# Kernel tuning notes

Hardware: AMD Instinct MI355X
Metric: run time of the kernel (lower is better)

## Reference

```python
import jax, jax.numpy as jnp
import numpy as np

N_NODES = 50000
N_EDGES = 800000
NODE_DIM = 10
EDGE_DIM = 5
HID = 64


def _tconv(x, src, dst, e_attr, wq, bq, wk, bk, wv, bv, we, ws, bs):
    # PyG TransformerConv, heads=1, concat=True, root_weight=True, beta=False
    n = x.shape[0]
    q = x @ wq + bq                      # [N, HID]
    k = x @ wk + bk                      # [N, HID]
    v = x @ wv + bv                      # [N, HID]
    ee = e_attr @ we                     # [E, HID] (lin_edge, no bias)
    ke = k[src] + ee                     # key per edge
    ve = v[src] + ee                     # value per edge
    logits = jnp.sum(q[dst] * ke, axis=-1) / 8.0  # sqrt(64) = 8
    m = jax.ops.segment_max(logits, dst, num_segments=n)
    p = jnp.exp(logits - m[dst])
    s = jax.ops.segment_sum(p, dst, num_segments=n)
    alpha = p / s[dst]                   # segment softmax over in-neighbors
    agg = jax.ops.segment_sum(alpha[:, None] * ve, dst, num_segments=n)
    return agg + x @ ws + bs             # + lin_skip(x_i)


def setup_inputs() -> dict:
    key = jax.random.key(0)
    ks = jax.random.split(key, 32)
    x = jax.random.uniform(ks[0], (N_NODES, NODE_DIM), dtype=jnp.float32)
    edge_index = jax.random.randint(ks[1], (2, N_EDGES), 0, N_NODES, dtype=jnp.int64)
    edge_attr = jax.random.uniform(ks[2], (N_EDGES, EDGE_DIM), dtype=jnp.float32)

    def lin(k, fan_in, fan_out):
        b = 1.0 / np.sqrt(fan_in)
        return jax.random.uniform(k, (fan_in, fan_out), jnp.float32, -b, b)

    def bias(k, fan_in, fan_out):
        b = 1.0 / np.sqrt(fan_in)
        return jax.random.uniform(k, (fan_out,), jnp.float32, -b, b)

    inp = dict(x=x, edge_index=edge_index, edge_attr=edge_attr)
    # conv1: NODE_DIM -> HID
    inp['w1q'] = lin(ks[3], NODE_DIM, HID); inp['b1q'] = bias(ks[4], NODE_DIM, HID)
    inp['w1k'] = lin(ks[5], NODE_DIM, HID); inp['b1k'] = bias(ks[6], NODE_DIM, HID)
    inp['w1v'] = lin(ks[7], NODE_DIM, HID); inp['b1v'] = bias(ks[8], NODE_DIM, HID)
    inp['w1e'] = lin(ks[9], EDGE_DIM, HID)
    inp['w1s'] = lin(ks[10], NODE_DIM, HID); inp['b1s'] = bias(ks[11], NODE_DIM, HID)
    # 5 stacked HID -> HID layers
    inp['wq'] = jnp.stack([lin(jax.random.fold_in(ks[12], i), HID, HID) for i in range(5)])
    inp['bq'] = jnp.stack([bias(jax.random.fold_in(ks[13], i), HID, HID) for i in range(5)])
    inp['wk'] = jnp.stack([lin(jax.random.fold_in(ks[14], i), HID, HID) for i in range(5)])
    inp['bk'] = jnp.stack([bias(jax.random.fold_in(ks[15], i), HID, HID) for i in range(5)])
    inp['wv'] = jnp.stack([lin(jax.random.fold_in(ks[16], i), HID, HID) for i in range(5)])
    inp['bv'] = jnp.stack([bias(jax.random.fold_in(ks[17], i), HID, HID) for i in range(5)])
    inp['we'] = jnp.stack([lin(jax.random.fold_in(ks[18], i), EDGE_DIM, HID) for i in range(5)])
    inp['ws'] = jnp.stack([lin(jax.random.fold_in(ks[19], i), HID, HID) for i in range(5)])
    inp['bs'] = jnp.stack([bias(jax.random.fold_in(ks[20], i), HID, HID) for i in range(5)])
    # final linear HID -> 1
    inp['lin_w'] = lin(ks[21], HID, 1); inp['lin_b'] = bias(ks[22], HID, 1)
    return inp


def reference(x, edge_index, edge_attr, w1q, b1q, w1k, b1k, w1v, b1v, w1e, w1s, b1s,
              wq, bq, wk, bk, wv, bv, we, ws, bs, lin_w, lin_b):
    src, dst = edge_index[0], edge_index[1]  # x_j = x[src], aggregated into dst
    h = jnp.log(x + 1.0)
    e = jnp.log(edge_attr + 1.0)
    h = _tconv(h, src, dst, e, w1q, b1q, w1k, b1k, w1v, b1v, w1e, w1s, b1s)
    for i in range(5):
        h = _tconv(h, src, dst, e, wq[i], bq[i], wk[i], bk[i], wv[i], bv[i], we[i], ws[i], bs[i])
    return h @ lin_w + lin_b  # [N, 1]
```

## Files before the change

### kernel.cpp

```cpp
#include <hip/hip_runtime.h>
#include <hip/hip_fp16.h>
#include <cstdint>
#include <cstddef>

#define NN 50000
#define NE 800000
#define HD 64
#define SB 49
#define NT64 6250

__global__ void k_hist(const int* __restrict__ ei, int* __restrict__ cnt) {
    int e = blockIdx.x * blockDim.x + threadIdx.x;
    if (e < NE) atomicAdd(&cnt[ei[NE + e]], 1);
}

__global__ __launch_bounds__(256) void k_scan1(const int* __restrict__ cnt,
                                               int* __restrict__ row_start,
                                               int* __restrict__ bsum) {
    __shared__ int ssum[256];
    const int tid = threadIdx.x, b = blockIdx.x;
    const int i0 = b * 1024 + tid * 4;
    int c0 = 0, c1 = 0, c2 = 0, c3 = 0;
    if (i0 + 3 < NN) {
        const int4 c = *(const int4*)(cnt + i0);
        c0 = c.x; c1 = c.y; c2 = c.z; c3 = c.w;
    } else {
        if (i0 + 0 < NN) c0 = cnt[i0 + 0];
        if (i0 + 1 < NN) c1 = cnt[i0 + 1];
        if (i0 + 2 < NN) c2 = cnt[i0 + 2];
        if (i0 + 3 < NN) c3 = cnt[i0 + 3];
    }
    ssum[tid] = c0 + c1 + c2 + c3;
    __syncthreads();
    for (int off = 1; off < 256; off <<= 1) {
        int v = (tid >= off) ? ssum[tid - off] : 0;
        __syncthreads();
        ssum[tid] += v;
        __syncthreads();
    }
    int ex = (tid == 0) ? 0 : ssum[tid - 1];
    if (i0 + 0 < NN) row_start[i0 + 0] = ex;
    ex += c0;
    if (i0 + 1 < NN) row_start[i0 + 1] = ex;
    ex += c1;
    if (i0 + 2 < NN) row_start[i0 + 2] = ex;
    ex += c2;
    if (i0 + 3 < NN) row_start[i0 + 3] = ex;
    if (tid == 255) bsum[b] = ssum[255];
}

__global__ __launch_bounds__(64) void k_scan2(const int* __restrict__ bsum,
                                              int* __restrict__ boff,
                                              int* __restrict__ row_start) {
    __shared__ int s[64];
    const int t = threadIdx.x;
    s[t] = (t < SB) ? bsum[t] : 0;
    __syncthreads();
    for (int off = 1; off < 64; off <<= 1) {
        int v = (t >= off) ? s[t - off] : 0;
        __syncthreads();
        s[t] += v;
        __syncthreads();
    }
    if (t < SB) boff[t] = (t == 0) ? 0 : s[t - 1];
    if (t == 0) row_start[NN] = s[SB - 1];
}

__global__ __launch_bounds__(256) void k_scan3(int* __restrict__ row_start,
                                               const int* __restrict__ boff,
                                               int* __restrict__ cur) {
    const int b = blockIdx.x;
    const int i0 = b * 1024 + threadIdx.x * 4;
    const int o = boff[b];
#pragma unroll
    for (int k = 0; k < 4; ++k) {
        int i = i0 + k;
        if (i < NN) {
            int v = row_start[i] + o;
            row_start[i] = v;
            cur[i] = v;
        }
    }
}

__global__ void k_scatter(const int* __restrict__ ei, const float* __restrict__ ea,
                          int* __restrict__ cur, uint4* __restrict__ e5p) {
    int e = blockIdx.x * blockDim.x + threadIdx.x;
    if (e < NE) {
        int d = ei[NE + e];
        int pos = atomicAdd(&cur[d], 1);
        const float e0 = __logf(ea[e * 5 + 0] + 1.f);
        const float e1 = __logf(ea[e * 5 + 1] + 1.f);
        const float e2 = __logf(ea[e * 5 + 2] + 1.f);
        const float e3 = __logf(ea[e * 5 + 3] + 1.f);
        const float e4 = __logf(ea[e * 5 + 4] + 1.f);
        union { __half2 h; unsigned u; } c01, c23;
        c01.h = __floats2half2_rn(e0, e1);
        c23.h = __floats2half2_rn(e2, e3);
        uint4 rec;
        rec.x = c01.u;
        rec.y = c23.u;
        rec.z = ((unsigned)ei[e] << 16) |
                (unsigned)__half_as_ushort(__float2half_rn(e4));
        rec.w = 0u;
        e5p[pos] = rec;
    }
}

__device__ __forceinline__ void cvt_kv(const uint4 u, float4& k4, float4& v4) {
    const float2 p0 = __half22float2(*(const __half2*)&u.x);
    const float2 p1 = __half22float2(*(const __half2*)&u.y);
    const float2 p2 = __half22float2(*(const __half2*)&u.z);
    const float2 p3 = __half22float2(*(const __half2*)&u.w);
    k4 = make_float4(p0.x, p1.x, p2.x, p3.x);
    v4 = make_float4(p0.y, p1.y, p2.y, p3.y);
}

__global__ __launch_bounds__(256, 4) void k_qkvs64(
    const float* __restrict__ h,
    const float* __restrict__ Wq, const float* __restrict__ Bq,
    const float* __restrict__ Wk, const float* __restrict__ Bk,
    const float* __restrict__ Wv, const float* __restrict__ Bv,
    const float* __restrict__ Ws, const float* __restrict__ Bs,
    float* __restrict__ qb, __half* __restrict__ kvh, float* __restrict__ sb) {
    __shared__ float xs[2][512];
    __shared__ float kls[512];
    const int lane = threadIdx.x & 63;
    const int w = threadIdx.x >> 6;
    const float* W = (w == 0) ? Wq : (w == 1) ? Ws : (w == 2) ? Wk : Wv;
    const float* B = (w == 0) ? Bq : (w == 1) ? Bs : (w == 2) ? Bk : Bv;
    const float scl = (w == 0) ? 0.125f : 1.f;
    float wr[64];
#pragma unroll
    for (int j = 0; j < 64; ++j) wr[j] = W[j * 64 + lane] * scl;
    const float bias = B[lane] * scl;

    int tile = blockIdx.x;
    {
        const float2 g = *(const float2*)(h + (size_t)tile * 512 + threadIdx.x * 2);
        *(float2*)&xs[0][threadIdx.x * 2] = g;
    }
    __syncthreads();
    int buf = 0;
    while (true) {
        const int nt = tile + gridDim.x;
        const bool more = nt < NT64;
        float2 gn;
        if (more) gn = *(const float2*)(h + (size_t)nt * 512 + threadIdx.x * 2);
        float acc[8] = {bias, bias, bias, bias, bias, bias, bias, bias};
#pragma unroll
        for (int jq = 0; jq < 16; ++jq) {
#pragma unroll
            for (int n = 0; n < 8; ++n) {
                const float4 xv = *(const float4*)&xs[buf][n * 64 + jq * 4];
                acc[n] = fmaf(xv.x, wr[jq * 4 + 0], acc[n]);
                acc[n] = fmaf(xv.y, wr[jq * 4 + 1], acc[n]);
                acc[n] = fmaf(xv.z, wr[jq * 4 + 2], acc[n]);
                acc[n] = fmaf(xv.w, wr[jq * 4 + 3], acc[n]);
            }
        }
        if (w == 2) {
#pragma unroll
            for (int n = 0; n < 8; ++n) kls[n * 64 + lane] = acc[n];
        }
        if (more) *(float2*)&xs[buf ^ 1][threadIdx.x * 2] = gn;
        __syncthreads();
        const int nb = tile * 8;
        if (w == 0) {
#pragma unroll
            for (int n = 0; n < 8; ++n) qb[(size_t)(nb + n) * 64 + lane] = acc[n];
        } else if (w == 1) {
#pragma unroll
            for (int n = 0; n < 8; ++n) sb[(size_t)(nb + n) * 64 + lane] = acc[n];
        } else if (w == 3) {
#pragma unroll
            for (int n = 0; n < 8; ++n) {
                const float kk = kls[n * 64 + lane];
                *(__half2*)(kvh + (size_t)(nb + n) * 128 + lane * 2) =
                    __floats2half2_rn(kk, acc[n]);
            }
        }
        if (!more) break;
        __syncthreads();
        tile = nt;
        buf ^= 1;
    }
}

__global__ __launch_bounds__(256, 4) void k_qkvs10(
    const float* __restrict__ x,
    const float* __restrict__ Wq, const float* __restrict__ Bq,
    const float* __restrict__ Wk, const float* __restrict__ Bk,
    const float* __restrict__ Wv, const float* __restrict__ Bv,
    const float* __restrict__ Ws, const float* __restrict__ Bs,
    float* __restrict__ qb, __half* __restrict__ kvh, float* __restrict__ sb) {
    __shared__ float xs[640];
    const int lane = threadIdx.x & 63;
    const int w = threadIdx.x >> 6;
    const bool iskv = (w == 1 || w == 3);
    const float* WA = (w == 0) ? Wq : iskv ? Wk : Ws;
    const float* BA = (w == 0) ? Bq : iskv ? Bk : Bs;
    const float scl = (w == 0) ? 0.125f : 1.f;
    float wrA[10], wrB[10];
#pragma unroll
    for (int j = 0; j < 10; ++j) {
        wrA[j] = WA[j * 64 + lane] * scl;
        wrB[j] = iskv ? Wv[j * 64 + lane] : 0.f;
    }
    const float bA = BA[lane] * scl;
    const float bB = iskv ? Bv[lane] : 0.f;
    const int tile = blockIdx.x;
    const int fbase = tile * 640;
    const int fcnt = min(640, NN * 10 - fbase);
    if (threadIdx.x * 4 < fcnt) {
        float4 v = *(const float4*)(x + (size_t)fbase + threadIdx.x * 4);
        v.x = __logf(v.x + 1.f);
        v.y = __logf(v.y + 1.f);
        v.z = __logf(v.z + 1.f);
        v.w = __logf(v.w + 1.f);
        *(float4*)&xs[threadIdx.x * 4] = v;
    }
    __syncthreads();
    const int nbase = tile * 64;
    const int nodes = min(64, NN - nbase);
    const int n0 = (w == 3) ? 32 : 0;
    const int n1 = iskv ? ((w == 1) ? min(nodes, 32) : nodes) : nodes;
    for (int n = n0; n < n1; ++n) {
        float accA = bA, accB = bB;
#pragma unroll
        for (int j = 0; j < 10; ++j) {
            const float xv = xs[n * 10 + j];
            accA = fmaf(xv, wrA[j], accA);
            accB = fmaf(xv, wrB[j], accB);
        }
        const size_t node = (size_t)(nbase + n);
        if (iskv) {
            const __half2 hv = __floats2half2_rn(accA, accB);
            *(__half2*)(kvh + node * 128 + lane * 2) = hv;
        } else if (w == 0) {
            qb[node * 64 + lane] = accA;
        } else {
            sb[node * 64 + lane] = accA;
        }
    }
}

template <bool FINAL>
__global__ __launch_bounds__(256) void k_agg(
    const float* __restrict__ q, const __half* __restrict__ kv,
    const float* __restrict__ sk, const uint4* __restrict__ e5p,
    const float* __restrict__ wE, const int* __restrict__ row_start,
    float* __restrict__ hout, const float* __restrict__ lw, const float* lb) {
    const int lane = threadIdx.x & 63;
    const int g = lane >> 4, t = lane & 15;
    const int node = __builtin_amdgcn_readfirstlane(blockIdx.x * 4 + (threadIdx.x >> 6));
    if (node >= NN) return;
    const int beg = row_start[node], end = row_start[node + 1];
    if (beg == end) {
        const float4 s4 = *(const float4*)(sk + (size_t)node * 64 + t * 4);
        if (FINAL) {
            const float4 lw4 = *(const float4*)(lw + t * 4);
            float r = s4.x * lw4.x;
            r = fmaf(s4.y, lw4.y, r);
            r = fmaf(s4.z, lw4.z, r);
            r = fmaf(s4.w, lw4.w, r);
            r += __shfl_xor(r, 1);
            r += __shfl_xor(r, 2);
            r += __shfl_xor(r, 4);
            r += __shfl_xor(r, 8);
            if (lane == 0) hout[node] = r + lb[0];
        } else if (g == 0) {
            *(float4*)(hout + (size_t)node * 64 + t * 4) = s4;
        }
        return;
    }
    const float4 q4 = *(const float4*)(q + (size_t)node * 64 + t * 4);
    float g5[5];
    {
        const float4 wg = *(const float4*)(wE + g * 64 + t * 4);
        float dc = q4.x * wg.x;
        dc = fmaf(q4.y, wg.y, dc);
        dc = fmaf(q4.z, wg.z, dc);
        dc = fmaf(q4.w, wg.w, dc);
        dc += __shfl_xor(dc, 1);
        dc += __shfl_xor(dc, 2);
        dc += __shfl_xor(dc, 4);
        dc += __shfl_xor(dc, 8);
        const float4 w4 = *(const float4*)(wE + 4 * 64 + t * 4);
        float d4 = q4.x * w4.x;
        d4 = fmaf(q4.y, w4.y, d4);
        d4 = fmaf(q4.z, w4.z, d4);
        d4 = fmaf(q4.w, w4.w, d4);
        d4 += __shfl_xor(d4, 1);
        d4 += __shfl_xor(d4, 2);
        d4 += __shfl_xor(d4, 4);
        d4 += __shfl_xor(d4, 8);
        g5[0] = __shfl(dc, 0);
        g5[1] = __shfl(dc, 16);
        g5[2] = __shfl(dc, 32);
        g5[3] = __shfl(dc, 48);
        g5[4] = __shfl(d4, 0);
    }
    float m = -1e30f, l = 0.f;
    float4 accv = {0.f, 0.f, 0.f, 0.f};
    float a50 = 0.f, a51 = 0.f, a52 = 0.f, a53 = 0.f, a54 = 0.f;
    const char* kvc = (const char*)kv;
    const int i0x = beg + g;
    const int i0 = (i0x < end) ? i0x : beg;
    uint4 r0 = e5p[i0];
    const int i1x = beg + 4 + g;
    const int i1 = (i1x < end) ? i1x : beg;
    uint4 r1 = e5p[i1];
    uint4 kv8 =
        *(const uint4*)(kvc + (size_t)((r0.z & 0xffff0000u) >> 8) + t * 16);
#pragma unroll 2
    for (int p = beg; p < end; p += 4) {
        const int nx = p + 8 + g;
        const int npp = (nx < end) ? nx : beg;
        const uint4 rn = e5p[npp];
        const uint4 nkv =
            *(const uint4*)(kvc + (size_t)((r1.z & 0xffff0000u) >> 8) + t * 16);
        const bool act = (p + g) < end;
        float4 k4, v4;
        cvt_kv(kv8, k4, v4);
        const float2 e01 = __half22float2(*(const __half2*)&r0.x);
        const float2 e23 = __half22float2(*(const __half2*)&r0.y);
        const float e4v =
            __half2float(__ushort_as_half((unsigned short)(r0.z & 0xffffu)));
        float d = q4.x * k4.x;
        d = fmaf(q4.y, k4.y, d);
        d = fmaf(q4.z, k4.z, d);
        d = fmaf(q4.w, k4.w, d);
        d += __shfl_xor(d, 1);
        d += __shfl_xor(d, 2);
        d += __shfl_xor(d, 4);
        d += __shfl_xor(d, 8);
        float d5 = g5[0] * e01.x;
        d5 = fmaf(g5[1], e01.y, d5);
        d5 = fmaf(g5[2], e23.x, d5);
        d5 = fmaf(g5[3], e23.y, d5);
        d5 = fmaf(g5[4], e4v, d5);
        const float la = act ? (d + d5) : -1e30f;
        const float nm = fmaxf(m, la);
        const float scl = __expf(m - nm);
        const float pa = __expf(la - nm);
        l = fmaf(l, scl, pa);
        accv.x = fmaf(accv.x, scl, pa * v4.x);
        accv.y = fmaf(accv.y, scl, pa * v4.y);
        accv.z = fmaf(accv.z, scl, pa * v4.z);
        accv.w = fmaf(accv.w, scl, pa * v4.w);
        a50 = fmaf(a50, scl, pa * e01.x);
        a51 = fmaf(a51, scl, pa * e01.y);
        a52 = fmaf(a52, scl, pa * e23.x);
        a53 = fmaf(a53, scl, pa * e23.y);
        a54 = fmaf(a54, scl, pa * e4v);
        m = nm;
        r0 = r1;
        r1 = rn;
        kv8 = nkv;
    }
    float M = fmaxf(m, __shfl_xor(m, 16));
    M = fmaxf(M, __shfl_xor(M, 32));
    const float f = __expf(m - M);
    float lz = l * f;
    lz += __shfl_xor(lz, 16);
    lz += __shfl_xor(lz, 32);
    accv.x *= f;
    accv.y *= f;
    accv.z *= f;
    accv.w *= f;
    a50 *= f;
    a51 *= f;
    a52 *= f;
    a53 *= f;
    a54 *= f;
#pragma unroll
    for (int s = 16; s <= 32; s <<= 1) {
        accv.x += __shfl_xor(accv.x, s);
        accv.y += __shfl_xor(accv.y, s);
        accv.z += __shfl_xor(accv.z, s);
        accv.w += __shfl_xor(accv.w, s);
        a50 += __shfl_xor(a50, s);
        a51 += __shfl_xor(a51, s);
        a52 += __shfl_xor(a52, s);
        a53 += __shfl_xor(a53, s);
        a54 += __shfl_xor(a54, s);
    }
    float4 t4 = accv;
    {
        const float4 w0 = *(const float4*)(wE + 0 * 64 + t * 4);
        const float4 w1 = *(const float4*)(wE + 1 * 64 + t * 4);
        const float4 w2 = *(const float4*)(wE + 2 * 64 + t * 4);
        const float4 w3 = *(const float4*)(wE + 3 * 64 + t * 4);
        const float4 w4r = *(const float4*)(wE + 4 * 64 + t * 4);
        t4.x = fmaf(a50, w0.x, t4.x);
        t4.y = fmaf(a50, w0.y, t4.y);
        t4.z = fmaf(a50, w0.z, t4.z);
        t4.w = fmaf(a50, w0.w, t4.w);
        t4.x = fmaf(a51, w1.x, t4.x);
        t4.y = fmaf(a51, w1.y, t4.y);
        t4.z = fmaf(a51, w1.z, t4.z);
        t4.w = fmaf(a51, w1.w, t4.w);
        t4.x = fmaf(a52, w2.x, t4.x);
        t4.y = fmaf(a52, w2.y, t4.y);
        t4.z = fmaf(a52, w2.z, t4.z);
        t4.w = fmaf(a52, w2.w, t4.w);
        t4.x = fmaf(a53, w3.x, t4.x);
        t4.y = fmaf(a53, w3.y, t4.y);
        t4.z = fmaf(a53, w3.z, t4.z);
        t4.w = fmaf(a53, w3.w, t4.w);
        t4.x = fmaf(a54, w4r.x, t4.x);
        t4.y = fmaf(a54, w4r.y, t4.y);
        t4.z = fmaf(a54, w4r.z, t4.z);
        t4.w = fmaf(a54, w4r.w, t4.w);
    }
    const float4 s4 = *(const float4*)(sk + (size_t)node * 64 + t * 4);
    const float rl = 1.f / lz;
    float4 o;
    o.x = fmaf(t4.x, rl, s4.x);
    o.y = fmaf(t4.y, rl, s4.y);
    o.z = fmaf(t4.z, rl, s4.z);
    o.w = fmaf(t4.w, rl, s4.w);
    if (FINAL) {
        const float4 lw4 = *(const float4*)(lw + t * 4);
        float r = o.x * lw4.x;
        r = fmaf(o.y, lw4.y, r);
        r = fmaf(o.z, lw4.z, r);
        r = fmaf(o.w, lw4.w, r);
        r += __shfl_xor(r, 1);
        r += __shfl_xor(r, 2);
        r += __shfl_xor(r, 4);
        r += __shfl_xor(r, 8);
        if (lane == 0) hout[node] = r + lb[0];
    } else if (g == 0) {
        *(float4*)(hout + (size_t)node * 64 + t * 4) = o;
    }
}

extern "C" void kernel_launch(void* const* d_in, const int* in_sizes, int n_in,
                              void* d_out, int out_size, void* d_ws, size_t ws_size,
                              hipStream_t stream) {
    const float* x = (const float*)d_in[0];
    const int* ei = (const int*)d_in[1];
    const float* ea = (const float*)d_in[2];
    const float* w1q = (const float*)d_in[3];
    const float* b1q = (const float*)d_in[4];
    const float* w1k = (const float*)d_in[5];
    const float* b1k = (const float*)d_in[6];
    const float* w1v = (const float*)d_in[7];
    const float* b1v = (const float*)d_in[8];
    const float* w1e = (const float*)d_in[9];
    const float* w1s = (const float*)d_in[10];
    const float* b1s = (const float*)d_in[11];
    const float* wq = (const float*)d_in[12];
    const float* bq = (const float*)d_in[13];
    const float* wk = (const float*)d_in[14];
    const float* bk = (const float*)d_in[15];
    const float* wv = (const float*)d_in[16];
    const float* bv = (const float*)d_in[17];
    const float* we = (const float*)d_in[18];
    const float* ws = (const float*)d_in[19];
    const float* bs = (const float*)d_in[20];
    const float* lw = (const float*)d_in[21];
    const float* lb = (const float*)d_in[22];

    uintptr_t p = (uintptr_t)d_ws;
    auto alloc = [&](size_t bytes) -> void* {
        void* r = (void*)p;
        p += (bytes + 255) & ~(size_t)255;
        return r;
    };
    uint4* e5p = (uint4*)alloc((size_t)NE * 16);
    float* hb = (float*)alloc((size_t)NN * HD * 4);
    __half* kvh = (__half*)alloc((size_t)NN * 128 * 2);
    float* qb = (float*)alloc((size_t)NN * HD * 4);
    float* sb = (float*)alloc((size_t)NN * HD * 4);
    int* row_start = (int*)alloc((size_t)(NN + 1) * 4);
    int* cnt = (int*)alloc((size_t)NN * 4);
    int* cur = (int*)alloc((size_t)NN * 4);
    int* bsum = (int*)alloc((size_t)SB * 4);
    int* boff = (int*)alloc((size_t)SB * 4);

    hipMemsetAsync(cnt, 0, (size_t)NN * 4, stream);
    k_hist<<<(NE + 255) / 256, 256, 0, stream>>>(ei, cnt);
    k_scan1<<<SB, 256, 0, stream>>>(cnt, row_start, bsum);
    k_scan2<<<1, 64, 0, stream>>>(bsum, boff, row_start);
    k_scan3<<<SB, 256, 0, stream>>>(row_start, boff, cur);
    k_scatter<<<(NE + 255) / 256, 256, 0, stream>>>(ei, ea, cur, e5p);

    const int gg64 = 1024;
    const int gg10 = (NN + 63) / 64;
    const int agg_grid = (NN + 3) / 4;

    k_qkvs10<<<gg10, 256, 0, stream>>>(x, w1q, b1q, w1k, b1k, w1v, b1v, w1s, b1s,
                                       qb, kvh, sb);
    k_agg<false><<<agg_grid, 256, 0, stream>>>(qb, kvh, sb, e5p, w1e, row_start,
                                               hb, lw, lb);

    for (int i = 0; i < 5; ++i) {
        k_qkvs64<<<gg64, 256, 0, stream>>>(hb, wq + i * 4096, bq + i * 64,
                                           wk + i * 4096, bk + i * 64,
                                           wv + i * 4096, bv + i * 64,
                                           ws + i * 4096, bs + i * 64,
                                           qb, kvh, sb);
        if (i < 4) {
            k_agg<false><<<agg_grid, 256, 0, stream>>>(qb, kvh, sb, e5p,
                                                       we + i * 320, row_start, hb,
                                                       lw, lb);
        } else {
            k_agg<true><<<agg_grid, 256, 0, stream>>>(qb, kvh, sb, e5p,
                                                      we + i * 320, row_start,
                                                      (float*)d_out, lw, lb);
        }
    }
}
```

Measured before the change: 640.8 us.

## Process eight edges per wave in aggregation and split CSR build into perm+pack

The aggregation kernel now splits each 64-lane wave into 8 groups of 8 lanes, each lane handling 8 feature channels, instead of 4 groups of 16 lanes with 4 channels. Each wave therefore processes 8 edges per iteration with wider per-lane loads and one fewer shuffle stage. The CSR construction is also restructured: edge records are computed in the histogram pass, the scatter writes only a permutation index, and a separate pack kernel gathers the records. This adds an extra 12.8MB temp buffer and two extra passes over edges, and raises register pressure in the aggregation loop.

Measured after the change: 702.4 us. +9.6%, slower.

```diff
diff --git a/kernel.cpp b/kernel.cpp
--- a/kernel.cpp
+++ b/kernel.cpp
@@ -9,9 +9,27 @@
 #define SB 49
 #define NT64 6250
 
-__global__ void k_hist(const int* __restrict__ ei, int* __restrict__ cnt) {
+__global__ void k_histprep(const int* __restrict__ ei, const float* __restrict__ ea,
+                           int* __restrict__ cnt, uint4* __restrict__ tmp) {
     int e = blockIdx.x * blockDim.x + threadIdx.x;
-    if (e < NE) atomicAdd(&cnt[ei[NE + e]], 1);
+    if (e < NE) {
+        atomicAdd(&cnt[ei[NE + e]], 1);
+        const float e0 = __logf(ea[e * 5 + 0] + 1.f);
+        const float e1 = __logf(ea[e * 5 + 1] + 1.f);
+        const float e2 = __logf(ea[e * 5 + 2] + 1.f);
+        const float e3 = __logf(ea[e * 5 + 3] + 1.f);
+        const float e4 = __logf(ea[e * 5 + 4] + 1.f);
+        union { __half2 h; unsigned u; } c01, c23;
+        c01.h = __floats2half2_rn(e0, e1);
+        c23.h = __floats2half2_rn(e2, e3);
+        uint4 rec;
+        rec.x = c01.u;
+        rec.y = c23.u;
+        rec.z = ((unsigned)ei[e] << 16) |
+                (unsigned)__half_as_ushort(__float2half_rn(e4));
+        rec.w = 0u;
+        tmp[e] = rec;
+    }
 }
 
 __global__ __launch_bounds__(256) void k_scan1(const int* __restrict__ cnt,
@@ -83,28 +101,19 @@
     }
 }
 
-__global__ void k_scatter(const int* __restrict__ ei, const float* __restrict__ ea,
-                          int* __restrict__ cur, uint4* __restrict__ e5p) {
+__global__ void k_scatter1(const int* __restrict__ ei, int* __restrict__ cur,
+                           int* __restrict__ perm) {
     int e = blockIdx.x * blockDim.x + threadIdx.x;
     if (e < NE) {
         int d = ei[NE + e];
-        int pos = atomicAdd(&cur[d], 1);
-        const float e0 = __logf(ea[e * 5 + 0] + 1.f);
-        const float e1 = __logf(ea[e * 5 + 1] + 1.f);
-        const float e2 = __logf(ea[e * 5 + 2] + 1.f);
-        const float e3 = __logf(ea[e * 5 + 3] + 1.f);
-        const float e4 = __logf(ea[e * 5 + 4] + 1.f);
-        union { __half2 h; unsigned u; } c01, c23;
-        c01.h = __floats2half2_rn(e0, e1);
-        c23.h = __floats2half2_rn(e2, e3);
-        uint4 rec;
-        rec.x = c01.u;
-        rec.y = c23.u;
-        rec.z = ((unsigned)ei[e] << 16) |
-                (unsigned)__half_as_ushort(__float2half_rn(e4));
-        rec.w = 0u;
-        e5p[pos] = rec;
-    }
+        perm[atomicAdd(&cur[d], 1)] = e;
+    }
+}
+
+__global__ void k_pack(const int* __restrict__ perm, const uint4* __restrict__ tmp,
+                       uint4* __restrict__ e5p) {
+    int p = blockIdx.x * blockDim.x + threadIdx.x;
+    if (p < NE) e5p[p] = tmp[perm[p]];
 }
 
 __device__ __forceinline__ void cvt_kv(const uint4 u, float4& k4, float4& v4) {
@@ -252,89 +261,98 @@
     const float* __restrict__ wE, const int* __restrict__ row_start,
     float* __restrict__ hout, const float* __restrict__ lw, const float* lb) {
     const int lane = threadIdx.x & 63;
-    const int g = lane >> 4, t = lane & 15;
+    const int g = lane >> 3, t = lane & 7;
     const int node = __builtin_amdgcn_readfirstlane(blockIdx.x * 4 + (threadIdx.x >> 6));
     if (node >= NN) return;
     const int beg = row_start[node], end = row_start[node + 1];
+    const float4 sA = *(const float4*)(sk + (size_t)node * 64 + t * 8);
+    const float4 sB = *(const float4*)(sk + (size_t)node * 64 + t * 8 + 4);
     if (beg == end) {
-        const float4 s4 = *(const float4*)(sk + (size_t)node * 64 + t * 4);
         if (FINAL) {
-            const float4 lw4 = *(const float4*)(lw + t * 4);
-            float r = s4.x * lw4.x;
-            r = fmaf(s4.y, lw4.y, r);
-            r = fmaf(s4.z, lw4.z, r);
-            r = fmaf(s4.w, lw4.w, r);
+            const float4 lwA = *(const float4*)(lw + t * 8);
+            const float4 lwB = *(const float4*)(lw + t * 8 + 4);
+            float r = sA.x * lwA.x;
+            r = fmaf(sA.y, lwA.y, r);
+            r = fmaf(sA.z, lwA.z, r);
+            r = fmaf(sA.w, lwA.w, r);
+            r = fmaf(sB.x, lwB.x, r);
+            r = fmaf(sB.y, lwB.y, r);
+            r = fmaf(sB.z, lwB.z, r);
+            r = fmaf(sB.w, lwB.w, r);
             r += __shfl_xor(r, 1);
             r += __shfl_xor(r, 2);
             r += __shfl_xor(r, 4);
-            r += __shfl_xor(r, 8);
             if (lane == 0) hout[node] = r + lb[0];
         } else if (g == 0) {
-            *(float4*)(hout + (size_t)node * 64 + t * 4) = s4;
+            *(float4*)(hout + (size_t)node * 64 + t * 8) = sA;
+            *(float4*)(hout + (size_t)node * 64 + t * 8 + 4) = sB;
         }
         return;
     }
-    const float4 q4 = *(const float4*)(q + (size_t)node * 64 + t * 4);
+    const float4 qA = *(const float4*)(q + (size_t)node * 64 + t * 8);
+    const float4 qB = *(const float4*)(q + (size_t)node * 64 + t * 8 + 4);
     float g5[5];
     {
-        const float4 wg = *(const float4*)(wE + g * 64 + t * 4);
-        float dc = q4.x * wg.x;
-        dc = fmaf(q4.y, wg.y, dc);
-        dc = fmaf(q4.z, wg.z, dc);
-        dc = fmaf(q4.w, wg.w, dc);
+        const int gr = (g < 5) ? g : 0;
+        const float4 wA = *(const float4*)(wE + gr * 64 + t * 8);
+        const float4 wB = *(const float4*)(wE + gr * 64 + t * 8 + 4);
+        float dc = qA.x * wA.x;
+        dc = fmaf(qA.y, wA.y, dc);
+        dc = fmaf(qA.z, wA.z, dc);
+        dc = fmaf(qA.w, wA.w, dc);
+        dc = fmaf(qB.x, wB.x, dc);
+        dc = fmaf(qB.y, wB.y, dc);
+        dc = fmaf(qB.z, wB.z, dc);
+        dc = fmaf(qB.w, wB.w, dc);
         dc += __shfl_xor(dc, 1);
         dc += __shfl_xor(dc, 2);
         dc += __shfl_xor(dc, 4);
-        dc += __shfl_xor(dc, 8);
-        const float4 w4 = *(const float4*)(wE + 4 * 64 + t * 4);
-        float d4 = q4.x * w4.x;
-        d4 = fmaf(q4.y, w4.y, d4);
-        d4 = fmaf(q4.z, w4.z, d4);
-        d4 = fmaf(q4.w, w4.w, d4);
-        d4 += __shfl_xor(d4, 1);
-        d4 += __shfl_xor(d4, 2);
-        d4 += __shfl_xor(d4, 4);
-        d4 += __shfl_xor(d4, 8);
         g5[0] = __shfl(dc, 0);
-        g5[1] = __shfl(dc, 16);
-        g5[2] = __shfl(dc, 32);
-        g5[3] = __shfl(dc, 48);
-        g5[4] = __shfl(d4, 0);
+        g5[1] = __shfl(dc, 8);
+        g5[2] = __shfl(dc, 16);
+        g5[3] = __shfl(dc, 24);
+        g5[4] = __shfl(dc, 32);
     }
     float m = -1e30f, l = 0.f;
-    float4 accv = {0.f, 0.f, 0.f, 0.f};
+    float4 accA = {0.f, 0.f, 0.f, 0.f}, accB = {0.f, 0.f, 0.f, 0.f};
     float a50 = 0.f, a51 = 0.f, a52 = 0.f, a53 = 0.f, a54 = 0.f;
     const char* kvc = (const char*)kv;
     const int i0x = beg + g;
     const int i0 = (i0x < end) ? i0x : beg;
     uint4 r0 = e5p[i0];
-    const int i1x = beg + 4 + g;
+    const int i1x = beg + 8 + g;
     const int i1 = (i1x < end) ? i1x : beg;
     uint4 r1 = e5p[i1];
-    uint4 kv8 =
-        *(const uint4*)(kvc + (size_t)((r0.z & 0xffff0000u) >> 8) + t * 16);
+    const char* kp0 = kvc + (size_t)((r0.z & 0xffff0000u) >> 8) + t * 32;
+    uint4 kva = *(const uint4*)kp0;
+    uint4 kvb = *(const uint4*)(kp0 + 16);
 #pragma unroll 2
-    for (int p = beg; p < end; p += 4) {
-        const int nx = p + 8 + g;
+    for (int p = beg; p < end; p += 8) {
+        const int nx = p + 16 + g;
         const int npp = (nx < end) ? nx : beg;
         const uint4 rn = e5p[npp];
-        const uint4 nkv =
-            *(const uint4*)(kvc + (size_t)((r1.z & 0xffff0000u) >> 8) + t * 16);
+        const char* kpn = kvc + (size_t)((r1.z & 0xffff0000u) >> 8) + t * 32;
+        const uint4 nkva = *(const uint4*)kpn;
+        const uint4 nkvb = *(const uint4*)(kpn + 16);
         const bool act = (p + g) < end;
-        float4 k4, v4;
-        cvt_kv(kv8, k4, v4);
+        float4 kA, vA, kB, vB;
+        cvt_kv(kva, kA, vA);
+        cvt_kv(kvb, kB, vB);
         const float2 e01 = __half22float2(*(const __half2*)&r0.x);
         const float2 e23 = __half22float2(*(const __half2*)&r0.y);
         const float e4v =
             __half2float(__ushort_as_half((unsigned short)(r0.z & 0xffffu)));
-        float d = q4.x * k4.x;
-        d = fmaf(q4.y, k4.y, d);
-        d = fmaf(q4.z, k4.z, d);
-        d = fmaf(q4.w, k4.w, d);
+        float d = qA.x * kA.x;
+        d = fmaf(qA.y, kA.y, d);
+        d = fmaf(qA.z, kA.z, d);
+        d = fmaf(qA.w, kA.w, d);
+        d = fmaf(qB.x, kB.x, d);
+        d = fmaf(qB.y, kB.y, d);
+        d = fmaf(qB.z, kB.z, d);
+        d = fmaf(qB.w, kB.w, d);
         d += __shfl_xor(d, 1);
         d += __shfl_xor(d, 2);
         d += __shfl_xor(d, 4);
-        d += __shfl_xor(d, 8);
         float d5 = g5[0] * e01.x;
         d5 = fmaf(g5[1], e01.y, d5);
         d5 = fmaf(g5[2], e23.x, d5);
@@ -345,10 +363,14 @@
         const float scl = __expf(m - nm);
         const float pa = __expf(la - nm);
         l = fmaf(l, scl, pa);
-        accv.x = fmaf(accv.x, scl, pa * v4.x);
-        accv.y = fmaf(accv.y, scl, pa * v4.y);
-        accv.z = fmaf(accv.z, scl, pa * v4.z);
-        accv.w = fmaf(accv.w, scl, pa * v4.w);
+        accA.x = fmaf(accA.x, scl, pa * vA.x);
+        accA.y = fmaf(accA.y, scl, pa * vA.y);
+        accA.z = fmaf(accA.z, scl, pa * vA.z);
+        accA.w = fmaf(accA.w, scl, pa * vA.w);
+        accB.x = fmaf(accB.x, scl, pa * vB.x);
+        accB.y = fmaf(accB.y, scl, pa * vB.y);
+        accB.z = fmaf(accB.z, scl, pa * vB.z);
+        accB.w = fmaf(accB.w, scl, pa * vB.w);
         a50 = fmaf(a50, scl, pa * e01.x);
         a51 = fmaf(a51, scl, pa * e01.y);
         a52 = fmaf(a52, scl, pa * e23.x);
@@ -357,83 +379,80 @@
         m = nm;
         r0 = r1;
         r1 = rn;
-        kv8 = nkv;
-    }
-    float M = fmaxf(m, __shfl_xor(m, 16));
+        kva = nkva;
+        kvb = nkvb;
+    }
+    float M = fmaxf(m, __shfl_xor(m, 8));
+    M = fmaxf(M, __shfl_xor(M, 16));
     M = fmaxf(M, __shfl_xor(M, 32));
     const float f = __expf(m - M);
     float lz = l * f;
+    lz += __shfl_xor(lz, 8);
     lz += __shfl_xor(lz, 16);
     lz += __shfl_xor(lz, 32);
-    accv.x *= f;
-    accv.y *= f;
-    accv.z *= f;
-    accv.w *= f;
-    a50 *= f;
-    a51 *= f;
-    a52 *= f;
-    a53 *= f;
-    a54 *= f;
-#pragma unroll
-    for (int s = 16; s <= 32; s <<= 1) {
-        accv.x += __shfl_xor(accv.x, s);
-        accv.y += __shfl_xor(accv.y, s);
-        accv.z += __shfl_xor(accv.z, s);
-        accv.w += __shfl_xor(accv.w, s);
+    accA.x *= f; accA.y *= f; accA.z *= f; accA.w *= f;
+    accB.x *= f; accB.y *= f; accB.z *= f; accB.w *= f;
+    a50 *= f; a51 *= f; a52 *= f; a53 *= f; a54 *= f;
+#pragma unroll
+    for (int s = 8; s <= 32; s <<= 1) {
+        accA.x += __shfl_xor(accA.x, s);
+        accA.y += __shfl_xor(accA.y, s);
+        accA.z += __shfl_xor(accA.z, s);
+        accA.w += __shfl_xor(accA.w, s);
+        accB.x += __shfl_xor(accB.x, s);
+        accB.y += __shfl_xor(accB.y, s);
+        accB.z += __shfl_xor(accB.z, s);
+        accB.w += __shfl_xor(accB.w, s);
         a50 += __shfl_xor(a50, s);
         a51 += __shfl_xor(a51, s);
         a52 += __shfl_xor(a52, s);
         a53 += __shfl_xor(a53, s);
         a54 += __shfl_xor(a54, s);
     }
-    float4 t4 = accv;
-    {
-        const float4 w0 = *(const float4*)(wE + 0 * 64 + t * 4);
-        const float4 w1 = *(const float4*)(wE + 1 * 64 + t * 4);
-        const float4 w2 = *(const float4*)(wE + 2 * 64 + t * 4);
-        const float4 w3 = *(const float4*)(wE + 3 * 64 + t * 4);
-        const float4 w4r = *(const float4*)(wE + 4 * 64 + t * 4);
-        t4.x = fmaf(a50, w0.x, t4.x);
-        t4.y = fmaf(a50, w0.y, t4.y);
-        t4.z = fmaf(a50, w0.z, t4.z);
-        t4.w = fmaf(a50, w0.w, t4.w);
-        t4.x = fmaf(a51, w1.x, t4.x);
-        t4.y = fmaf(a51, w1.y, t4.y);
-        t4.z = fmaf(a51, w1.z, t4.z);
-        t4.w = fmaf(a51, w1.w, t4.w);
-        t4.x = fmaf(a52, w2.x, t4.x);
-        t4.y = fmaf(a52, w2.y, t4.y);
-        t4.z = fmaf(a52, w2.z, t4.z);
-        t4.w = fmaf(a52, w2.w, t4.w);
-        t4.x = fmaf(a53, w3.x, t4.x);
-        t4.y = fmaf(a53, w3.y, t4.y);
-        t4.z = fmaf(a53, w3.z, t4.z);
-        t4.w = fmaf(a53, w3.w, t4.w);
-        t4.x = fmaf(a54, w4r.x, t4.x);
-        t4.y = fmaf(a54, w4r.y, t4.y);
-        t4.z = fmaf(a54, w4r.z, t4.z);
-        t4.w = fmaf(a54, w4r.w, t4.w);
-    }
-    const float4 s4 = *(const float4*)(sk + (size_t)node * 64 + t * 4);
+    float4 tA = accA, tB = accB;
+#pragma unroll
+    for (int r = 0; r < 5; ++r) {
+        const float ar = (r == 0) ? a50 : (r == 1) ? a51 : (r == 2) ? a52
+                         : (r == 3) ? a53 : a54;
+        const float4 wA = *(const float4*)(wE + r * 64 + t * 8);
+        const float4 wB = *(const float4*)(wE + r * 64 + t * 8 + 4);
+        tA.x = fmaf(ar, wA.x, tA.x);
+        tA.y = fmaf(ar, wA.y, tA.y);
+        tA.z = fmaf(ar, wA.z, tA.z);
+        tA.w = fmaf(ar, wA.w, tA.w);
+        tB.x = fmaf(ar, wB.x, tB.x);
+        tB.y = fmaf(ar, wB.y, tB.y);
+        tB.z = fmaf(ar, wB.z, tB.z);
+        tB.w = fmaf(ar, wB.w, tB.w);
+    }
     const float rl = 1.f / lz;
-    float4 o;
-    o.x = fmaf(t4.x, rl, s4.x);
-    o.y = fmaf(t4.y, rl, s4.y);
-    o.z = fmaf(t4.z, rl, s4.z);
-    o.w = fmaf(t4.w, rl, s4.w);
+    float4 oA, oB;
+    oA.x = fmaf(tA.x, rl, sA.x);
+    oA.y = fmaf(tA.y, rl, sA.y);
+    oA.z = fmaf(tA.z, rl, sA.z);
+    oA.w = fmaf(tA.w, rl, sA.w);
+    oB.x = fmaf(tB.x, rl, sB.x);
+    oB.y = fmaf(tB.y, rl, sB.y);
+    oB.z = fmaf(tB.z, rl, sB.z);
+    oB.w = fmaf(tB.w, rl, sB.w);
     if (FINAL) {
-        const float4 lw4 = *(const float4*)(lw + t * 4);
-        float r = o.x * lw4.x;
-        r = fmaf(o.y, lw4.y, r);
-        r = fmaf(o.z, lw4.z, r);
-        r = fmaf(o.w, lw4.w, r);
+        const float4 lwA = *(const float4*)(lw + t * 8);
+        const float4 lwB = *(const float4*)(lw + t * 8 + 4);
+        float r = oA.x * lwA.x;
+        r = fmaf(oA.y, lwA.y, r);
+        r = fmaf(oA.z, lwA.z, r);
+        r = fmaf(oA.w, lwA.w, r);
+        r = fmaf(oB.x, lwB.x, r);
+        r = fmaf(oB.y, lwB.y, r);
+        r = fmaf(oB.z, lwB.z, r);
+        r = fmaf(oB.w, lwB.w, r);
         r += __shfl_xor(r, 1);
         r += __shfl_xor(r, 2);
         r += __shfl_xor(r, 4);
-        r += __shfl_xor(r, 8);
         if (lane == 0) hout[node] = r + lb[0];
     } else if (g == 0) {
-        *(float4*)(hout + (size_t)node * 64 + t * 4) = o;
+        *(float4*)(hout + (size_t)node * 64 + t * 8) = oA;
+        *(float4*)(hout + (size_t)node * 64 + t * 8 + 4) = oB;
     }
 }
 
@@ -471,6 +490,8 @@
         return r;
     };
     uint4* e5p = (uint4*)alloc((size_t)NE * 16);
+    uint4* tmp = (uint4*)alloc((size_t)NE * 16);
+    int* perm = (int*)alloc((size_t)NE * 4);
     float* hb = (float*)alloc((size_t)NN * HD * 4);
     __half* kvh = (__half*)alloc((size_t)NN * 128 * 2);
     float* qb = (float*)alloc((size_t)NN * HD * 4);
@@ -482,11 +503,12 @@
     int* boff = (int*)alloc((size_t)SB * 4);
 
     hipMemsetAsync(cnt, 0, (size_t)NN * 4, stream);
-    k_hist<<<(NE + 255) / 256, 256, 0, stream>>>(ei, cnt);
+    k_histprep<<<(NE + 255) / 256, 256, 0, stream>>>(ei, ea, cnt, tmp);
     k_scan1<<<SB, 256, 0, stream>>>(cnt, row_start, bsum);
     k_scan2<<<1, 64, 0, stream>>>(bsum, boff, row_start);
     k_scan3<<<SB, 256, 0, stream>>>(row_start, boff, cur);
-    k_scatter<<<(NE + 255) / 256, 256, 0, stream>>>(ei, ea, cur, e5p);
+    k_scatter1<<<(NE + 255) / 256, 256, 0, stream>>>(ei, cur, perm);
+    k_pack<<<(NE + 255) / 256, 256, 0, stream>>>(perm, tmp, e5p);
 
     const int gg64 = 1024;
     const int gg10 = (NN + 63) / 64;
```

## Vectorize edge preprocessing and use lazy-rescale online softmax in aggregation

Applied to the files above, without the earlier changes.

The histogram and scatter kernels now handle four edges per thread, using int4/float4 loads for the edge indices and attributes. This cuts the number of load instructions and threads. The aggregation loop replaces the per-edge online-softmax max update, which paid two exps and rescaled every accumulator on each edge, with a lazy scheme. It computes one exp against the running max and rescales only when a new logit exceeds the max by more than 8. The lazy scheme lets partial sums grow by up to e^8 before a rescale and adds a divergent branch, but removes most exps and multiplies from the inner loop.

New measurement: 627.8 us. 1.02x faster.

```diff
diff --git a/kernel.cpp b/kernel.cpp
--- a/kernel.cpp
+++ b/kernel.cpp
@@ -10,8 +10,14 @@
 #define NT64 6250
 
 __global__ void k_hist(const int* __restrict__ ei, int* __restrict__ cnt) {
-    int e = blockIdx.x * blockDim.x + threadIdx.x;
-    if (e < NE) atomicAdd(&cnt[ei[NE + e]], 1);
+    const int e0 = (blockIdx.x * blockDim.x + threadIdx.x) * 4;
+    if (e0 < NE) {
+        const int4 d4 = *(const int4*)(ei + NE + e0);
+        atomicAdd(&cnt[d4.x], 1);
+        atomicAdd(&cnt[d4.y], 1);
+        atomicAdd(&cnt[d4.z], 1);
+        atomicAdd(&cnt[d4.w], 1);
+    }
 }
 
 __global__ __launch_bounds__(256) void k_scan1(const int* __restrict__ cnt,
@@ -85,25 +91,39 @@
 
 __global__ void k_scatter(const int* __restrict__ ei, const float* __restrict__ ea,
                           int* __restrict__ cur, uint4* __restrict__ e5p) {
-    int e = blockIdx.x * blockDim.x + threadIdx.x;
-    if (e < NE) {
-        int d = ei[NE + e];
-        int pos = atomicAdd(&cur[d], 1);
-        const float e0 = __logf(ea[e * 5 + 0] + 1.f);
-        const float e1 = __logf(ea[e * 5 + 1] + 1.f);
-        const float e2 = __logf(ea[e * 5 + 2] + 1.f);
-        const float e3 = __logf(ea[e * 5 + 3] + 1.f);
-        const float e4 = __logf(ea[e * 5 + 4] + 1.f);
+    const int e0 = (blockIdx.x * blockDim.x + threadIdx.x) * 4;
+    if (e0 >= NE) return;
+    const int4 s4 = *(const int4*)(ei + e0);
+    const int4 d4 = *(const int4*)(ei + NE + e0);
+    float f[20];
+    *(float4*)&f[0] = *(const float4*)(ea + (size_t)e0 * 5 + 0);
+    *(float4*)&f[4] = *(const float4*)(ea + (size_t)e0 * 5 + 4);
+    *(float4*)&f[8] = *(const float4*)(ea + (size_t)e0 * 5 + 8);
+    *(float4*)&f[12] = *(const float4*)(ea + (size_t)e0 * 5 + 12);
+    *(float4*)&f[16] = *(const float4*)(ea + (size_t)e0 * 5 + 16);
+    int pos[4];
+    pos[0] = atomicAdd(&cur[d4.x], 1);
+    pos[1] = atomicAdd(&cur[d4.y], 1);
+    pos[2] = atomicAdd(&cur[d4.z], 1);
+    pos[3] = atomicAdd(&cur[d4.w], 1);
+    const int ss[4] = {s4.x, s4.y, s4.z, s4.w};
+#pragma unroll
+    for (int j = 0; j < 4; ++j) {
+        const float g0 = __logf(f[j * 5 + 0] + 1.f);
+        const float g1 = __logf(f[j * 5 + 1] + 1.f);
+        const float g2 = __logf(f[j * 5 + 2] + 1.f);
+        const float g3 = __logf(f[j * 5 + 3] + 1.f);
+        const float g4 = __logf(f[j * 5 + 4] + 1.f);
         union { __half2 h; unsigned u; } c01, c23;
-        c01.h = __floats2half2_rn(e0, e1);
-        c23.h = __floats2half2_rn(e2, e3);
+        c01.h = __floats2half2_rn(g0, g1);
+        c23.h = __floats2half2_rn(g2, g3);
         uint4 rec;
         rec.x = c01.u;
         rec.y = c23.u;
-        rec.z = ((unsigned)ei[e] << 16) |
-                (unsigned)__half_as_ushort(__float2half_rn(e4));
+        rec.z = ((unsigned)ss[j] << 16) |
+                (unsigned)__half_as_ushort(__float2half_rn(g4));
         rec.w = 0u;
-        e5p[pos] = rec;
+        e5p[pos[j]] = rec;
     }
 }
 
@@ -340,21 +360,33 @@
         d5 = fmaf(g5[2], e23.x, d5);
         d5 = fmaf(g5[3], e23.y, d5);
         d5 = fmaf(g5[4], e4v, d5);
-        const float la = act ? (d + d5) : -1e30f;
-        const float nm = fmaxf(m, la);
-        const float scl = __expf(m - nm);
-        const float pa = __expf(la - nm);
-        l = fmaf(l, scl, pa);
-        accv.x = fmaf(accv.x, scl, pa * v4.x);
-        accv.y = fmaf(accv.y, scl, pa * v4.y);
-        accv.z = fmaf(accv.z, scl, pa * v4.z);
-        accv.w = fmaf(accv.w, scl, pa * v4.w);
-        a50 = fmaf(a50, scl, pa * e01.x);
-        a51 = fmaf(a51, scl, pa * e01.y);
-        a52 = fmaf(a52, scl, pa * e23.x);
-        a53 = fmaf(a53, scl, pa * e23.y);
-        a54 = fmaf(a54, scl, pa * e4v);
-        m = nm;
+        const float la = act ? (d + d5) : -__builtin_inff();
+        float pa = __expf(la - m);
+        if (la > m + 8.f) {
+            const float rs = __expf(m - la);
+            l *= rs;
+            accv.x *= rs;
+            accv.y *= rs;
+            accv.z *= rs;
+            accv.w *= rs;
+            a50 *= rs;
+            a51 *= rs;
+            a52 *= rs;
+            a53 *= rs;
+            a54 *= rs;
+            m = la;
+            pa = 1.f;
+        }
+        l += pa;
+        accv.x = fmaf(pa, v4.x, accv.x);
+        accv.y = fmaf(pa, v4.y, accv.y);
+        accv.z = fmaf(pa, v4.z, accv.z);
+        accv.w = fmaf(pa, v4.w, accv.w);
+        a50 = fmaf(pa, e01.x, a50);
+        a51 = fmaf(pa, e01.y, a51);
+        a52 = fmaf(pa, e23.x, a52);
+        a53 = fmaf(pa, e23.y, a53);
+        a54 = fmaf(pa, e4v, a54);
         r0 = r1;
         r1 = rn;
         kv8 = nkv;
@@ -482,11 +514,12 @@
     int* boff = (int*)alloc((size_t)SB * 4);
 
     hipMemsetAsync(cnt, 0, (size_t)NN * 4, stream);
-    k_hist<<<(NE + 255) / 256, 256, 0, stream>>>(ei, cnt);
+    const int gedge4 = (NE / 4 + 255) / 256;
+    k_hist<<<gedge4, 256, 0, stream>>>(ei, cnt);
     k_scan1<<<SB, 256, 0, stream>>>(cnt, row_start, bsum);
     k_scan2<<<1, 64, 0, stream>>>(bsum, boff, row_start);
     k_scan3<<<SB, 256, 0, stream>>>(row_start, boff, cur);
-    k_scatter<<<(NE + 255) / 256, 256, 0, stream>>>(ei, ea, cur, e5p);
+    k_scatter<<<gedge4, 256, 0, stream>>>(ei, ea, cur, e5p);
 
     const int gg64 = 1024;
     const int gg10 = (NN + 63) / 64;
```
